# Performance work log

Hardware: AMD Instinct MI355X
Metric: run time of the kernel (lower is better)

## Reference

```python
import jax, jax.numpy as jnp
import numpy as np

DIM_IN, DIM_OUT, DIM_HID = 1024, 1024, 1024
BATCH = 16384


def setup_inputs() -> dict:
    key = jax.random.key(0)
    k1, k2, k3, k4 = jax.random.split(key, 4)
    x = jax.random.normal(k1, (BATCH, DIM_IN), dtype=jnp.float32)
    # W_slow: Linear(dim_in -> dim_out + 2*dim_hidden + 1)
    W_slow_w = jax.random.normal(k2, (DIM_OUT + 2 * DIM_HID + 1, DIM_IN), dtype=jnp.float32) * (1.0 / np.sqrt(DIM_IN))
    W_slow_b = jax.random.normal(k3, (DIM_OUT + 2 * DIM_HID + 1,), dtype=jnp.float32) * 0.01
    # W_fast: Linear(dim_hidden -> dim_out), weight initialized to zero per module
    W_fast_w = jnp.zeros((DIM_OUT, DIM_HID), dtype=jnp.float32)
    W_fast_b = jax.random.normal(k4, (DIM_OUT,), dtype=jnp.float32) * 0.01
    return {"x": x, "W_slow_w": W_slow_w, "W_slow_b": W_slow_b,
            "W_fast_w": W_fast_w, "W_fast_b": W_fast_b}


def reference(x, W_slow_w, W_slow_b, W_fast_w, W_fast_b):
    B = x.shape[0]
    s = x @ W_slow_w.T + W_slow_b                      # [B, O + 2H + 1]
    k = s[:, :DIM_HID]                                 # [B, H]
    v = s[:, DIM_HID:DIM_HID + DIM_OUT]                # [B, O]
    q = s[:, DIM_HID + DIM_OUT:DIM_HID + DIM_OUT + DIM_HID]  # [B, H]
    lr = jax.nn.sigmoid(s[:, -1:])                     # [B, 1]
    # fast-weight read with softmax key
    v_bar = jax.nn.softmax(k, axis=1) @ W_fast_w.T + W_fast_b  # [B, O]
    # delta-rule outer-product update (batched, normalized by B)
    delta = jnp.einsum('bo,bh->oh', lr * (v - v_bar), jax.nn.sigmoid(k)) / B  # [O, H]
    W_new = W_fast_w + delta
    # read with updated fast weights
    return jax.nn.softmax(q, axis=1) @ W_new.T + W_fast_b  # [B, O]
```

## Files before the change

### kernel.cpp

```cpp
#include <hip/hip_runtime.h>
#include <math.h>

static constexpr int BATCH = 16384;

typedef __attribute__((ext_vector_type(8))) __bf16 bf16x8;
typedef __attribute__((ext_vector_type(4))) float f32x4;

__device__ __forceinline__ float sigm(float x) { return 1.0f / (1.0f + expf(-x)); }

__device__ __forceinline__ unsigned short f2bf(float f) {
  unsigned u = __float_as_uint(f);
  return (unsigned short)((u + 0x7fffu + ((u >> 16) & 1u)) >> 16);
}
__device__ __forceinline__ float bf2f(unsigned short u) {
  return __uint_as_float((unsigned)u << 16);
}

template <int EPI>
__global__ __launch_bounds__(256) void mgemm(
    const unsigned short* __restrict__ Ag, const unsigned short* __restrict__ Bg,
    int lda, int ldb, int ksl, const float* __restrict__ bias,
    unsigned short* __restrict__ t0, unsigned short* __restrict__ t1,
    unsigned short* __restrict__ t2, float* __restrict__ Cf,
    const unsigned short* __restrict__ vTin, const float* __restrict__ lrp,
    unsigned short* __restrict__ outT, int ldT) {
  __shared__ unsigned short As[128 * 32];
  __shared__ unsigned short Bs[128 * 32];
  const int tid = threadIdx.x, lane = tid & 63, w = tid >> 6;
  const int lm = lane & 15, kg = lane >> 4;
  const int mh = (w >> 1) * 64, nh = (w & 1) * 64;
  const int bm = blockIdx.y * 128, bn = blockIdx.x * 128;
  const int kstart = blockIdx.z * ksl, kend = kstart + ksl;
  f32x4 acc[4][4] = {};

  int offA[4], offB[4];
#pragma unroll
  for (int i = 0; i < 4; i++) {
    int rA = mh + i * 16 + lm;
    offA[i] = rA * 32 + (((kg + rA + (rA >> 2)) & 3) << 3);
    int rB = nh + i * 16 + lm;
    offB[i] = rB * 32 + (((kg + rB + (rB >> 2)) & 3) << 3);
  }
  int rowS[2], kcS[2];
#pragma unroll
  for (int t = 0; t < 2; t++) {
    int c = (w * 2 + t) * 64 + lane;
    rowS[t] = c >> 2;
    kcS[t] = ((((c & 3) - rowS[t] - (rowS[t] >> 2)) & 3) << 3);
  }

  for (int k0 = kstart; k0 < kend; k0 += 32) {
#pragma unroll
    for (int t = 0; t < 2; t++) {
      __builtin_amdgcn_global_load_lds(
          (__attribute__((address_space(1))) void*)(unsigned short*)(
              Ag + (size_t)(bm + rowS[t]) * lda + k0 + kcS[t]),
          (__attribute__((address_space(3))) void*)(As + (w * 2 + t) * 512), 16, 0, 0);
      __builtin_amdgcn_global_load_lds(
          (__attribute__((address_space(1))) void*)(unsigned short*)(
              Bg + (size_t)(bn + rowS[t]) * ldb + k0 + kcS[t]),
          (__attribute__((address_space(3))) void*)(Bs + (w * 2 + t) * 512), 16, 0, 0);
    }
    __syncthreads();
    bf16x8 aF[4], bF[4];
#pragma unroll
    for (int i = 0; i < 4; i++) {
      aF[i] = *(const bf16x8*)(As + offA[i]);
      bF[i] = *(const bf16x8*)(Bs + offB[i]);
    }
#pragma unroll
    for (int i = 0; i < 4; i++)
#pragma unroll
      for (int j = 0; j < 4; j++)
        acc[i][j] = __builtin_amdgcn_mfma_f32_16x16x32_bf16(aF[i], bF[j], acc[i][j], 0, 0, 0);
    __syncthreads();
  }

#pragma unroll
  for (int i = 0; i < 4; i++) {
#pragma unroll
    for (int j = 0; j < 4; j++) {
      const int gcol = bn + nh + j * 16 + lm;
      const int grow0 = bm + mh + i * 16 + kg * 4;
      if (EPI == 0) {
        const int which = gcol >> 10;
        unsigned short* dst = which == 0 ? t0 : (which == 1 ? t1 : t2);
        const float bv = bias[gcol];
        ushort4 pk;
        pk.x = f2bf(acc[i][j][0] + bv);
        pk.y = f2bf(acc[i][j][1] + bv);
        pk.z = f2bf(acc[i][j][2] + bv);
        pk.w = f2bf(acc[i][j][3] + bv);
        *(ushort4*)(dst + (size_t)(gcol & 1023) * ldT + grow0) = pk;
      } else if (EPI == 1) {
        const float bv = bias[gcol];
        const float4 l4 = *(const float4*)(lrp + grow0);
        const ushort4 v4 = *(const ushort4*)(vTin + (size_t)gcol * ldT + grow0);
        ushort4 o;
        o.x = f2bf(l4.x * (bf2f(v4.x) - (acc[i][j][0] + bv)));
        o.y = f2bf(l4.y * (bf2f(v4.y) - (acc[i][j][1] + bv)));
        o.z = f2bf(l4.z * (bf2f(v4.z) - (acc[i][j][2] + bv)));
        o.w = f2bf(l4.w * (bf2f(v4.w) - (acc[i][j][3] + bv)));
        *(ushort4*)(outT + (size_t)gcol * ldT + grow0) = o;
      } else if (EPI == 2) {
        const float bv = bias[gcol];
#pragma unroll
        for (int r = 0; r < 4; r++)
          Cf[(size_t)(grow0 + r) * 1024 + gcol] = acc[i][j][r] + bv;
      } else {
        float* dst = Cf + (size_t)blockIdx.z * (1024ull * 1024ull);
#pragma unroll
        for (int r = 0; r < 4; r++)
          dst[(size_t)(grow0 + r) * 1024 + gcol] = acc[i][j][r];
      }
    }
  }
}

template <bool DOSIG>
__global__ __launch_bounds__(256) void tsoftmax(
    const unsigned short* __restrict__ in, int ldin,
    unsigned short* __restrict__ rowout,
    unsigned short* __restrict__ sigT, int ldT) {
  __shared__ unsigned short tile[1024 * 16];
  __shared__ float red[16 * 17];
  const int t = threadIdx.x, bl = t & 15, fg = t >> 4;
  const int B0 = blockIdx.x * 16;
  const int f0 = fg * 64;
  float ls = 0.f;
  for (int f = f0; f < f0 + 64; f++) {
    unsigned short u = in[(size_t)f * ldin + B0 + bl];
    tile[f * 16 + bl] = u;
    ls += expf(bf2f(u));
  }
  red[bl * 17 + fg] = ls;
  __syncthreads();
  float tot = 0.f;
#pragma unroll
  for (int g = 0; g < 16; g++) tot += red[bl * 17 + g];
  const float inv = 1.0f / tot;
  for (int fb = f0; fb < f0 + 64; fb += 4) {
    float v[4];
#pragma unroll
    for (int e = 0; e < 4; e++) v[e] = bf2f(tile[(fb + e) * 16 + bl]);
    ushort4 o;
    o.x = f2bf(expf(v[0]) * inv);
    o.y = f2bf(expf(v[1]) * inv);
    o.z = f2bf(expf(v[2]) * inv);
    o.w = f2bf(expf(v[3]) * inv);
    *(ushort4*)(rowout + (size_t)(B0 + bl) * 1024 + fb) = o;
    if (DOSIG) {
#pragma unroll
      for (int e = 0; e < 4; e++)
        sigT[(size_t)(fb + e) * ldT + B0 + bl] = f2bf(sigm(v[e]));
    }
  }
}

__global__ __launch_bounds__(256) void lrx(const float* __restrict__ x,
                                           const float* __restrict__ Wsw,
                                           const float* __restrict__ Wsb,
                                           float* __restrict__ lrOut,
                                           unsigned short* __restrict__ xbf) {
  const int lane = threadIdx.x & 63, w = threadIdx.x >> 6;
  const int b = blockIdx.x * 4 + w;
  const float* xr = x + (size_t)b * 1024;
  const float* wr = Wsw + 3072ull * 1024ull;
  float sum = 0.f;
#pragma unroll
  for (int j = 0; j < 4; j++) {
    int f = lane + 64 * j;
    float4 xv = ((const float4*)xr)[f];
    float4 wv = ((const float4*)wr)[f];
    sum += xv.x * wv.x + xv.y * wv.y + xv.z * wv.z + xv.w * wv.w;
    ushort4 o = {f2bf(xv.x), f2bf(xv.y), f2bf(xv.z), f2bf(xv.w)};
    ((ushort4*)(xbf + (size_t)b * 1024))[f] = o;
  }
#pragma unroll
  for (int o = 32; o; o >>= 1) sum += __shfl_down(sum, o, 64);
  if (lane == 0) lrOut[b] = sigm(sum + Wsb[3072]);
}

__global__ __launch_bounds__(256) void cvt_bf(const float* __restrict__ in,
                                              unsigned short* __restrict__ outp) {
  size_t i = (size_t)blockIdx.x * 256 + threadIdx.x;
  float4 v = ((const float4*)in)[i];
  ushort4 o = {f2bf(v.x), f2bf(v.y), f2bf(v.z), f2bf(v.w)};
  ((ushort4*)outp)[i] = o;
}

__global__ __launch_bounds__(256) void wnewk(const float* __restrict__ P,
                                             const float* __restrict__ Wfw,
                                             unsigned short* __restrict__ wnbf) {
  const size_t i = (size_t)blockIdx.x * 256 + threadIdx.x;
  float s = 0.f;
#pragma unroll
  for (int z = 0; z < 8; z++) s += P[(size_t)z * (1024ull * 1024ull) + i];
  wnbf[i] = f2bf(Wfw[i] + s * (1.0f / 16384.0f));
}

extern "C" void kernel_launch(void* const* d_in, const int* in_sizes, int n_in,
                              void* d_out, int out_size, void* d_ws, size_t ws_size,
                              hipStream_t stream) {
  (void)in_sizes; (void)n_in; (void)out_size;
  const float* x   = (const float*)d_in[0];
  const float* Wsw = (const float*)d_in[1];
  const float* Wsb = (const float*)d_in[2];
  const float* Wfw = (const float*)d_in[3];
  const float* Wfb = (const float*)d_in[4];
  float* out = (float*)d_out;

  const size_t MB = 1ull << 20;
  int nc;
  if      (ws_size >= 216 * MB) nc = 1;
  else if (ws_size >= 164 * MB) nc = 2;
  else if (ws_size >= 122 * MB) nc = 4;
  else                          nc = 8;
  const size_t Bc = BATCH / nc;
  const int BcI = (int)Bc;
  const int zc = 8 / nc;
  const size_t CB = Bc * 1024 * 2;

  char* p = (char*)d_ws;
  size_t off = 0;
  auto alloc = [&](size_t bytes) {
    char* cur = p + off;
    off = (off + bytes + 255) & ~(size_t)255;
    return cur;
  };
  unsigned short* wbf  = (unsigned short*)alloc(3072ull * 1024 * 2);
  unsigned short* wfbf = (unsigned short*)alloc(1024ull * 1024 * 2);
  unsigned short* wnbf = (unsigned short*)alloc(1024ull * 1024 * 2);
  float*          lr   = (float*)alloc(BATCH * 4);
  unsigned short* qsm  = (unsigned short*)alloc((size_t)BATCH * 1024 * 2);

  unsigned short *xbf, *ksm, *kt, *Ut, *vT, *qt, *SKt;
  float* P;
  if (nc == 1) {
    char* rA = alloc(CB);
    char* rB = alloc(CB);
    char* rC = alloc(CB);
    char* rD = alloc(CB);
    char* rE = alloc(CB);
    xbf = (unsigned short*)rA; ksm = (unsigned short*)rA;
    kt  = (unsigned short*)rB; Ut  = (unsigned short*)rB;
    vT  = (unsigned short*)rC;
    qt  = (unsigned short*)rD; P   = (float*)rD;
    SKt = (unsigned short*)rE;
  } else {
    P   = (float*)alloc(32 * MB);
    char* rA = alloc(CB);
    char* rB = alloc(CB);
    xbf = (unsigned short*)rA; ksm = (unsigned short*)rA;
    kt  = (unsigned short*)rB; Ut  = (unsigned short*)rB;
    vT  = (unsigned short*)alloc(CB);
    qt  = (unsigned short*)alloc(CB);
    SKt = (unsigned short*)alloc(CB);
  }

  cvt_bf<<<dim3(3072), 256, 0, stream>>>(Wsw, wbf);
  cvt_bf<<<dim3(1024), 256, 0, stream>>>(Wfw, wfbf);

  for (int c = 0; c < nc; c++) {
    const float* xc = x + (size_t)c * Bc * 1024;
    float* lrc = lr + (size_t)c * Bc;
    lrx<<<dim3((unsigned)(Bc / 4)), 256, 0, stream>>>(xc, Wsw, Wsb, lrc, xbf);
    mgemm<0><<<dim3(24, Bc / 128), 256, 0, stream>>>(
        xbf, wbf, 1024, 1024, 1024, Wsb, kt, vT, qt, nullptr, nullptr,
        nullptr, nullptr, BcI);
    tsoftmax<true><<<dim3((unsigned)(Bc / 16)), 256, 0, stream>>>(
        kt, BcI, ksm, SKt, BcI);
    tsoftmax<false><<<dim3((unsigned)(Bc / 16)), 256, 0, stream>>>(
        qt, BcI, qsm + (size_t)c * Bc * 1024, nullptr, BcI);
    mgemm<1><<<dim3(8, Bc / 128), 256, 0, stream>>>(
        ksm, wfbf, 1024, 1024, 1024, Wfb, nullptr, nullptr, nullptr, nullptr,
        vT, lrc, Ut, BcI);
    mgemm<3><<<dim3(8, 8, zc), 256, 0, stream>>>(
        Ut, SKt, BcI, BcI, 2048, nullptr, nullptr, nullptr, nullptr,
        P + (size_t)c * zc * 1024 * 1024, nullptr, nullptr, nullptr, BcI);
  }

  wnewk<<<dim3(1024 * 1024 / 256), 256, 0, stream>>>(P, Wfw, wnbf);

  mgemm<2><<<dim3(8, BATCH / 128), 256, 0, stream>>>(
      qsm, wnbf, 1024, 1024, 1024, Wfb, nullptr, nullptr, nullptr, out,
      nullptr, nullptr, nullptr, 0);
}
```

Measured before the change: 572.8 us.

## Add 256x256 tile GEMM with 4-stage LDS pipeline for K=1024 GEMMs

Introduces mgemm8, a 512-thread kernel computing 256x256 output tiles with a four-buffer LDS ring and prefetch two k-steps ahead. It splits the A fragment loads into two halves interleaved with async global-to-LDS staging, and uses explicit waitcnt, barriers and setprio to overlap memory with MFMA. The three big K=1024 GEMMs (projection, fast-weight read, final read) switch to it, while the split-K outer-product GEMM keeps the old kernel. Larger tiles raise data reuse and reduce the number of blocks, at the cost of 128KB of LDS per block and higher register pressure.

Measured after the change: 511.6 us. 1.12x faster.

```diff
diff --git a/kernel.cpp b/kernel.cpp
--- a/kernel.cpp
+++ b/kernel.cpp
@@ -17,71 +17,115 @@
 }
 
 template <int EPI>
-__global__ __launch_bounds__(256) void mgemm(
+__global__ __launch_bounds__(512, 2) void mgemm8(
     const unsigned short* __restrict__ Ag, const unsigned short* __restrict__ Bg,
-    int lda, int ldb, int ksl, const float* __restrict__ bias,
+    int lda, int ldb, const float* __restrict__ bias,
     unsigned short* __restrict__ t0, unsigned short* __restrict__ t1,
     unsigned short* __restrict__ t2, float* __restrict__ Cf,
     const unsigned short* __restrict__ vTin, const float* __restrict__ lrp,
     unsigned short* __restrict__ outT, int ldT) {
-  __shared__ unsigned short As[128 * 32];
-  __shared__ unsigned short Bs[128 * 32];
+  constexpr int NT = 32;
+  __shared__ unsigned short As[4 * 8192];
+  __shared__ unsigned short Bs[4 * 8192];
   const int tid = threadIdx.x, lane = tid & 63, w = tid >> 6;
   const int lm = lane & 15, kg = lane >> 4;
-  const int mh = (w >> 1) * 64, nh = (w & 1) * 64;
-  const int bm = blockIdx.y * 128, bn = blockIdx.x * 128;
-  const int kstart = blockIdx.z * ksl, kend = kstart + ksl;
-  f32x4 acc[4][4] = {};
-
-  int offA[4], offB[4];
-#pragma unroll
-  for (int i = 0; i < 4; i++) {
-    int rA = mh + i * 16 + lm;
-    offA[i] = rA * 32 + (((kg + rA + (rA >> 2)) & 3) << 3);
-    int rB = nh + i * 16 + lm;
-    offB[i] = rB * 32 + (((kg + rB + (rB >> 2)) & 3) << 3);
-  }
-  int rowS[2], kcS[2];
-#pragma unroll
-  for (int t = 0; t < 2; t++) {
-    int c = (w * 2 + t) * 64 + lane;
-    rowS[t] = c >> 2;
-    kcS[t] = ((((c & 3) - rowS[t] - (rowS[t] >> 2)) & 3) << 3);
-  }
-
-  for (int k0 = kstart; k0 < kend; k0 += 32) {
-#pragma unroll
-    for (int t = 0; t < 2; t++) {
+  const int wm = w >> 2, wn = w & 3;
+  const int bm = blockIdx.y * 256, bn = blockIdx.x * 256;
+  f32x4 acc[8][4] = {};
+
+  int offA[8], offB[4];
+#pragma unroll
+  for (int i = 0; i < 8; i++) {
+    int r = wm * 128 + i * 16 + lm;
+    offA[i] = r * 32 + (((kg + r + (r >> 2)) & 3) << 3);
+  }
+#pragma unroll
+  for (int j = 0; j < 4; j++) {
+    int r = wn * 64 + j * 16 + lm;
+    offB[j] = r * 32 + (((kg + r + (r >> 2)) & 3) << 3);
+  }
+  const unsigned short* gA[2];
+  const unsigned short* gB[2];
+  int ldsoff[2];
+#pragma unroll
+  for (int i = 0; i < 2; i++) {
+    int r = i * 128 + w * 16 + (lane >> 2);
+    int q = ((lane & 3) - r - (r >> 2)) & 3;
+    gA[i] = Ag + (size_t)(bm + r) * lda + q * 8;
+    gB[i] = Bg + (size_t)(bn + r) * ldb + q * 8;
+    ldsoff[i] = i * 4096 + w * 512;
+  }
+  auto stageA = [&](int tt, int buf) {
+#pragma unroll
+    for (int i = 0; i < 2; i++)
       __builtin_amdgcn_global_load_lds(
-          (__attribute__((address_space(1))) void*)(unsigned short*)(
-              Ag + (size_t)(bm + rowS[t]) * lda + k0 + kcS[t]),
-          (__attribute__((address_space(3))) void*)(As + (w * 2 + t) * 512), 16, 0, 0);
+          (__attribute__((address_space(1))) void*)(unsigned short*)(gA[i] + tt * 32),
+          (__attribute__((address_space(3))) void*)(As + buf * 8192 + ldsoff[i]),
+          16, 0, 0);
+  };
+  auto stageB = [&](int tt, int buf) {
+#pragma unroll
+    for (int i = 0; i < 2; i++)
       __builtin_amdgcn_global_load_lds(
-          (__attribute__((address_space(1))) void*)(unsigned short*)(
-              Bg + (size_t)(bn + rowS[t]) * ldb + k0 + kcS[t]),
-          (__attribute__((address_space(3))) void*)(Bs + (w * 2 + t) * 512), 16, 0, 0);
-    }
-    __syncthreads();
+          (__attribute__((address_space(1))) void*)(unsigned short*)(gB[i] + tt * 32),
+          (__attribute__((address_space(3))) void*)(Bs + buf * 8192 + ldsoff[i]),
+          16, 0, 0);
+  };
+
+  stageA(0, 0); stageB(0, 0);
+  stageA(1, 1); stageB(1, 1);
+  asm volatile("s_waitcnt vmcnt(4)" ::: "memory");
+  __builtin_amdgcn_s_barrier();
+  __builtin_amdgcn_sched_barrier(0);
+
+  for (int t = 0; t < NT; ++t) {
+    const unsigned short* Ab = As + (t & 3) * 8192;
+    const unsigned short* Bb = Bs + (t & 3) * 8192;
     bf16x8 aF[4], bF[4];
 #pragma unroll
-    for (int i = 0; i < 4; i++) {
-      aF[i] = *(const bf16x8*)(As + offA[i]);
-      bF[i] = *(const bf16x8*)(Bs + offB[i]);
-    }
+    for (int i = 0; i < 4; i++) aF[i] = *(const bf16x8*)(Ab + offA[i]);
+#pragma unroll
+    for (int j = 0; j < 4; j++) bF[j] = *(const bf16x8*)(Bb + offB[j]);
+    if (t + 2 < NT) stageA(t + 2, (t + 2) & 3);
+    __builtin_amdgcn_s_barrier();
+    asm volatile("s_waitcnt lgkmcnt(0)" ::: "memory");
+    __builtin_amdgcn_sched_barrier(0);
+    __builtin_amdgcn_s_setprio(1);
 #pragma unroll
     for (int i = 0; i < 4; i++)
 #pragma unroll
       for (int j = 0; j < 4; j++)
         acc[i][j] = __builtin_amdgcn_mfma_f32_16x16x32_bf16(aF[i], bF[j], acc[i][j], 0, 0, 0);
-    __syncthreads();
-  }
-
-#pragma unroll
-  for (int i = 0; i < 4; i++) {
+    __builtin_amdgcn_s_setprio(0);
+    __builtin_amdgcn_sched_barrier(0);
+    __builtin_amdgcn_s_barrier();
+    bf16x8 aG[4];
+#pragma unroll
+    for (int i = 0; i < 4; i++) aG[i] = *(const bf16x8*)(Ab + offA[4 + i]);
+    if (t + 2 < NT) stageB(t + 2, (t + 2) & 3);
+    __builtin_amdgcn_s_barrier();
+    asm volatile("s_waitcnt lgkmcnt(0)" ::: "memory");
+    __builtin_amdgcn_sched_barrier(0);
+    __builtin_amdgcn_s_setprio(1);
+#pragma unroll
+    for (int i = 0; i < 4; i++)
+#pragma unroll
+      for (int j = 0; j < 4; j++)
+        acc[4 + i][j] = __builtin_amdgcn_mfma_f32_16x16x32_bf16(aG[i], bF[j], acc[4 + i][j], 0, 0, 0);
+    __builtin_amdgcn_s_setprio(0);
+    __builtin_amdgcn_sched_barrier(0);
+    if (t < NT - 2) { asm volatile("s_waitcnt vmcnt(4)" ::: "memory"); }
+    else            { asm volatile("s_waitcnt vmcnt(0)" ::: "memory"); }
+    __builtin_amdgcn_s_barrier();
+    __builtin_amdgcn_sched_barrier(0);
+  }
+
+#pragma unroll
+  for (int i = 0; i < 8; i++) {
 #pragma unroll
     for (int j = 0; j < 4; j++) {
-      const int gcol = bn + nh + j * 16 + lm;
-      const int grow0 = bm + mh + i * 16 + kg * 4;
+      const int gcol = bn + wn * 64 + j * 16 + lm;
+      const int grow0 = bm + wm * 128 + i * 16 + kg * 4;
       if (EPI == 0) {
         const int which = gcol >> 10;
         unsigned short* dst = which == 0 ? t0 : (which == 1 ? t1 : t2);
@@ -102,12 +146,83 @@
         o.z = f2bf(l4.z * (bf2f(v4.z) - (acc[i][j][2] + bv)));
         o.w = f2bf(l4.w * (bf2f(v4.w) - (acc[i][j][3] + bv)));
         *(ushort4*)(outT + (size_t)gcol * ldT + grow0) = o;
-      } else if (EPI == 2) {
+      } else {
         const float bv = bias[gcol];
 #pragma unroll
         for (int r = 0; r < 4; r++)
           Cf[(size_t)(grow0 + r) * 1024 + gcol] = acc[i][j][r] + bv;
-      } else {
+      }
+    }
+  }
+}
+
+template <int EPI>
+__global__ __launch_bounds__(256) void mgemm(
+    const unsigned short* __restrict__ Ag, const unsigned short* __restrict__ Bg,
+    int lda, int ldb, int ksl, const float* __restrict__ bias,
+    unsigned short* __restrict__ t0, unsigned short* __restrict__ t1,
+    unsigned short* __restrict__ t2, float* __restrict__ Cf,
+    const unsigned short* __restrict__ vTin, const float* __restrict__ lrp,
+    unsigned short* __restrict__ outT, int ldT) {
+  __shared__ unsigned short As[128 * 32];
+  __shared__ unsigned short Bs[128 * 32];
+  const int tid = threadIdx.x, lane = tid & 63, w = tid >> 6;
+  const int lm = lane & 15, kg = lane >> 4;
+  const int mh = (w >> 1) * 64, nh = (w & 1) * 64;
+  const int bm = blockIdx.y * 128, bn = blockIdx.x * 128;
+  const int kstart = blockIdx.z * ksl, kend = kstart + ksl;
+  f32x4 acc[4][4] = {};
+
+  int offA[4], offB[4];
+#pragma unroll
+  for (int i = 0; i < 4; i++) {
+    int rA = mh + i * 16 + lm;
+    offA[i] = rA * 32 + (((kg + rA + (rA >> 2)) & 3) << 3);
+    int rB = nh + i * 16 + lm;
+    offB[i] = rB * 32 + (((kg + rB + (rB >> 2)) & 3) << 3);
+  }
+  int rowS[2], kcS[2];
+#pragma unroll
+  for (int t = 0; t < 2; t++) {
+    int c = (w * 2 + t) * 64 + lane;
+    rowS[t] = c >> 2;
+    kcS[t] = ((((c & 3) - rowS[t] - (rowS[t] >> 2)) & 3) << 3);
+  }
+
+  for (int k0 = kstart; k0 < kend; k0 += 32) {
+#pragma unroll
+    for (int t = 0; t < 2; t++) {
+      __builtin_amdgcn_global_load_lds(
+          (__attribute__((address_space(1))) void*)(unsigned short*)(
+              Ag + (size_t)(bm + rowS[t]) * lda + k0 + kcS[t]),
+          (__attribute__((address_space(3))) void*)(As + (w * 2 + t) * 512), 16, 0, 0);
+      __builtin_amdgcn_global_load_lds(
+          (__attribute__((address_space(1))) void*)(unsigned short*)(
+              Bg + (size_t)(bn + rowS[t]) * ldb + k0 + kcS[t]),
+          (__attribute__((address_space(3))) void*)(Bs + (w * 2 + t) * 512), 16, 0, 0);
+    }
+    __syncthreads();
+    bf16x8 aF[4], bF[4];
+#pragma unroll
+    for (int i = 0; i < 4; i++) {
+      aF[i] = *(const bf16x8*)(As + offA[i]);
+      bF[i] = *(const bf16x8*)(Bs + offB[i]);
+    }
+#pragma unroll
+    for (int i = 0; i < 4; i++)
+#pragma unroll
+      for (int j = 0; j < 4; j++)
+        acc[i][j] = __builtin_amdgcn_mfma_f32_16x16x32_bf16(aF[i], bF[j], acc[i][j], 0, 0, 0);
+    __syncthreads();
+  }
+
+#pragma unroll
+  for (int i = 0; i < 4; i++) {
+#pragma unroll
+    for (int j = 0; j < 4; j++) {
+      const int gcol = bn + nh + j * 16 + lm;
+      const int grow0 = bm + mh + i * 16 + kg * 4;
+      if (EPI == 3) {
         float* dst = Cf + (size_t)blockIdx.z * (1024ull * 1024ull);
 #pragma unroll
         for (int r = 0; r < 4; r++)
@@ -265,15 +380,15 @@
     const float* xc = x + (size_t)c * Bc * 1024;
     float* lrc = lr + (size_t)c * Bc;
     lrx<<<dim3((unsigned)(Bc / 4)), 256, 0, stream>>>(xc, Wsw, Wsb, lrc, xbf);
-    mgemm<0><<<dim3(24, Bc / 128), 256, 0, stream>>>(
-        xbf, wbf, 1024, 1024, 1024, Wsb, kt, vT, qt, nullptr, nullptr,
-        nullptr, nullptr, BcI);
+    mgemm8<0><<<dim3(12, (unsigned)(Bc / 256)), 512, 0, stream>>>(
+        xbf, wbf, 1024, 1024, Wsb, kt, vT, qt, nullptr, nullptr, nullptr,
+        nullptr, BcI);
     tsoftmax<true><<<dim3((unsigned)(Bc / 16)), 256, 0, stream>>>(
         kt, BcI, ksm, SKt, BcI);
     tsoftmax<false><<<dim3((unsigned)(Bc / 16)), 256, 0, stream>>>(
         qt, BcI, qsm + (size_t)c * Bc * 1024, nullptr, BcI);
-    mgemm<1><<<dim3(8, Bc / 128), 256, 0, stream>>>(
-        ksm, wfbf, 1024, 1024, 1024, Wfb, nullptr, nullptr, nullptr, nullptr,
+    mgemm8<1><<<dim3(4, (unsigned)(Bc / 256)), 512, 0, stream>>>(
+        ksm, wfbf, 1024, 1024, Wfb, nullptr, nullptr, nullptr, nullptr,
         vT, lrc, Ut, BcI);
     mgemm<3><<<dim3(8, 8, zc), 256, 0, stream>>>(
         Ut, SKt, BcI, BcI, 2048, nullptr, nullptr, nullptr, nullptr,
@@ -282,7 +397,7 @@
 
   wnewk<<<dim3(1024 * 1024 / 256), 256, 0, stream>>>(P, Wfw, wnbf);
 
-  mgemm<2><<<dim3(8, BATCH / 128), 256, 0, stream>>>(
-      qsm, wnbf, 1024, 1024, 1024, Wfb, nullptr, nullptr, nullptr, out,
+  mgemm8<2><<<dim3(4, BATCH / 256), 512, 0, stream>>>(
+      qsm, wnbf, 1024, 1024, Wfb, nullptr, nullptr, nullptr, out,
       nullptr, nullptr, nullptr, 0);
 }
```
